# Optimization experiments

Hardware: AMD Instinct MI355X
Metric: run time of the kernel (lower is better)

## Reference

```python
import jax, jax.numpy as jnp
import numpy as np

D = 8  # polynomial degree; with bias present, basis has D columns (P1..PD)


def setup_inputs() -> dict:
    key = jax.random.key(0)
    k1, k2 = jax.random.split(key)
    batch, n_in, n_out = 65536, 256, 64
    x = jax.random.normal(k1, (batch, n_in), dtype=jnp.float32)
    c_basis = jax.random.normal(k2, (n_out, n_in, D), dtype=jnp.float32) * (1.0 / np.sqrt(n_in * D))
    bias = jnp.zeros((n_out,), dtype=jnp.float32)
    return {"x": x, "c_basis": c_basis, "bias": bias}


def _legendre_basis(x):
    # x: (batch, n_in). Returns (batch, n_in, D) = [P1(t), ..., PD(t)], t = tanh(x).
    t = jnp.tanh(x)
    p_prev = jnp.ones_like(t)  # P0
    p_curr = t                 # P1
    polys = [p_curr]
    for k in range(2, D + 1):  # small fixed-length loop over degree
        p_next = ((2 * k - 1) * t * p_curr - (k - 1) * p_prev) / k
        polys.append(p_next)
        p_prev, p_curr = p_curr, p_next
    return jnp.stack(polys, axis=-1)  # (batch, n_in, D)


def reference(x, c_basis, bias):
    # basis: (batch, n_in, D); contract over (n_in, D) with c_basis (n_out, n_in, D)
    leg = _legendre_basis(x)
    y = jnp.einsum('bid,oid->bo', leg, c_basis)
    return y + bias
```

## Files before the change

### kernel.cpp

```cpp
#include <hip/hip_runtime.h>
#include <hip/hip_bf16.h>

typedef _Float16 half2v __attribute__((ext_vector_type(2)));
typedef _Float16 half8 __attribute__((ext_vector_type(8)));
typedef __attribute__((ext_vector_type(4))) float floatx4;
typedef __attribute__((ext_vector_type(4))) unsigned int uintx4;

#define GLOBAL_AS __attribute__((address_space(1)))
#define LDS_AS __attribute__((address_space(3)))

__device__ __forceinline__ void async_ld16(const void* g, void* l) {
  __builtin_amdgcn_global_load_lds((const GLOBAL_AS unsigned int*)g,
                                   (LDS_AS unsigned int*)l, 16, 0, 0);
}

__device__ __forceinline__ half2v h2(float v) {
  return (half2v){(_Float16)v, (_Float16)v};
}

__device__ __forceinline__ void legendre2_f16(float xv0, float xv1,
                                              half8* fa0, half8* fa1) {
  float e0 = __builtin_amdgcn_exp2f(xv0 * 2.885390081777927f);
  float t0 = 1.0f - 2.0f * __builtin_amdgcn_rcpf(e0 + 1.0f);
  float e1 = __builtin_amdgcn_exp2f(xv1 * 2.885390081777927f);
  float t1 = 1.0f - 2.0f * __builtin_amdgcn_rcpf(e1 + 1.0f);
  half2v t;
  { auto tt = __builtin_amdgcn_cvt_pkrtz(t0, t1); __builtin_memcpy(&t, &tt, 4); }
  half2v p1 = t;
  half2v u2 = t * p1, w2 = u2 - h2(1.0f);  half2v p2 = h2(0.5f)      * w2 + u2;
  half2v u3 = t * p2, w3 = u3 - p1;        half2v p3 = h2(2.0f/3.0f) * w3 + u3;
  half2v u4 = t * p3, w4 = u4 - p2;        half2v p4 = h2(0.75f)     * w4 + u4;
  half2v u5 = t * p4, w5 = u5 - p3;        half2v p5 = h2(0.8f)      * w5 + u5;
  half2v u6 = t * p5, w6 = u6 - p4;        half2v p6 = h2(5.0f/6.0f) * w6 + u6;
  half2v u7 = t * p6, w7 = u7 - p5;        half2v p7 = h2(6.0f/7.0f) * w7 + u7;
  half2v u8 = t * p7, w8 = u8 - p6;        half2v p8 = h2(7.0f/8.0f) * w8 + u8;
  unsigned P[8];
  __builtin_memcpy(&P[0], &p1, 4); __builtin_memcpy(&P[1], &p2, 4);
  __builtin_memcpy(&P[2], &p3, 4); __builtin_memcpy(&P[3], &p4, 4);
  __builtin_memcpy(&P[4], &p5, 4); __builtin_memcpy(&P[5], &p6, 4);
  __builtin_memcpy(&P[6], &p7, 4); __builtin_memcpy(&P[7], &p8, 4);
  union { unsigned u[4]; half8 h; } a0, a1;
#pragma unroll
  for (int j = 0; j < 4; ++j) {
    a0.u[j] = __builtin_amdgcn_perm(P[2*j+1], P[2*j], 0x05040100u);
    a1.u[j] = __builtin_amdgcn_perm(P[2*j+1], P[2*j], 0x07060302u);
  }
  *fa0 = a0.h;
  *fa1 = a1.h;
}

__global__ void conv_kernel(const float* __restrict__ cb, _Float16* __restrict__ ws) {
  int t = blockIdx.x * 128 + threadIdx.x;
  int o = t >> 8;
  int i = t & 255;
  const floatx4* s = (const floatx4*)(cb + ((size_t)o * 256 + i) * 8);
  floatx4 v0 = s[0], v1 = s[1];
  union { _Float16 h[8]; uintx4 u; } w;
  w.h[0] = (_Float16)v0.x; w.h[1] = (_Float16)v0.y;
  w.h[2] = (_Float16)v0.z; w.h[3] = (_Float16)v0.w;
  w.h[4] = (_Float16)v1.x; w.h[5] = (_Float16)v1.y;
  w.h[6] = (_Float16)v1.z; w.h[7] = (_Float16)v1.w;
  *(uintx4*)(ws + (size_t)i * 512 + o * 8) = w.u;
}

#define NCH 16

__global__ __launch_bounds__(128, 2) void kan_kernel(
    const float* __restrict__ x, const _Float16* __restrict__ ws,
    const float* __restrict__ bias, float* __restrict__ y) {
  __shared__ __align__(16) _Float16 bt[2][16 * 64 * 8];

  const int tid  = threadIdx.x;
  const int wid  = tid >> 6;
  const int lane = tid & 63;
  const int m    = lane & 15;
  const int q    = lane >> 4;
  const int row_block = blockIdx.x * 64;

  floatx4 acc[2][4];
#pragma unroll
  for (int a = 0; a < 2; ++a)
#pragma unroll
    for (int nt = 0; nt < 4; ++nt) acc[a][nt] = (floatx4){0.f, 0.f, 0.f, 0.f};

  const _Float16* bsrc[8];
#pragma unroll
  for (int t = 0; t < 8; ++t)
    bsrc[t] = ws + (size_t)(t * 128 + wid * 64 + lane) * 8;

  const float* xp0 = x + (size_t)(row_block + wid * 32 + m) * 256 + q * 4;
  const float* xp1 = xp0 + 16 * 256;

  floatx4 xa0 = *(const floatx4*)xp0;
  floatx4 xa1 = *(const floatx4*)xp1;
  floatx4 xb0 = *(const floatx4*)(xp0 + 16);
  floatx4 xb1 = *(const floatx4*)(xp1 + 16);
  xp0 += 32; xp1 += 32;

  auto stage = [&](int b) {
#pragma unroll
    for (int t = 0; t < 8; ++t) {
      int sb = t * 128 + wid * 64;
      async_ld16(bsrc[t], &bt[b][sb * 8]);
      bsrc[t] += 8192;
    }
  };

  stage(0);

#pragma unroll 2
  for (int ch = 0; ch < NCH; ++ch) {
    const int buf = ch & 1;

    half8 f0[4], f1[4];
#pragma unroll
    for (int j = 0; j < 4; ++j)
      legendre2_f16(xa0[j], xa1[j], &f0[j], &f1[j]);

    asm volatile("s_barrier" ::: "memory");

    floatx4 xn0 = xb0, xn1 = xb1;
    if (ch + 1 < NCH) {
      stage(buf ^ 1);
      if (ch + 2 < NCH) {
        xn0 = *(const floatx4*)xp0;
        xn1 = *(const floatx4*)xp1;
        xp0 += 16; xp1 += 16;
      }
      asm volatile("s_waitcnt vmcnt(10)" ::: "memory");
    } else {
      asm volatile("s_waitcnt vmcnt(0)" ::: "memory");
    }
    asm volatile("s_barrier" ::: "memory");

    __builtin_amdgcn_s_setprio(1);
    const _Float16* bp = &bt[buf][q * 2048 + m * 8];
#pragma unroll
    for (int j = 0; j < 4; ++j) {
      half8 fb0 = *(const half8*)(bp + j * 512 + 0 * 128);
      half8 fb1 = *(const half8*)(bp + j * 512 + 1 * 128);
      half8 fb2 = *(const half8*)(bp + j * 512 + 2 * 128);
      half8 fb3 = *(const half8*)(bp + j * 512 + 3 * 128);
      acc[0][0] = __builtin_amdgcn_mfma_f32_16x16x32_f16(f0[j], fb0, acc[0][0], 0, 0, 0);
      acc[1][0] = __builtin_amdgcn_mfma_f32_16x16x32_f16(f1[j], fb0, acc[1][0], 0, 0, 0);
      acc[0][1] = __builtin_amdgcn_mfma_f32_16x16x32_f16(f0[j], fb1, acc[0][1], 0, 0, 0);
      acc[1][1] = __builtin_amdgcn_mfma_f32_16x16x32_f16(f1[j], fb1, acc[1][1], 0, 0, 0);
      acc[0][2] = __builtin_amdgcn_mfma_f32_16x16x32_f16(f0[j], fb2, acc[0][2], 0, 0, 0);
      acc[1][2] = __builtin_amdgcn_mfma_f32_16x16x32_f16(f1[j], fb2, acc[1][2], 0, 0, 0);
      acc[0][3] = __builtin_amdgcn_mfma_f32_16x16x32_f16(f0[j], fb3, acc[0][3], 0, 0, 0);
      acc[1][3] = __builtin_amdgcn_mfma_f32_16x16x32_f16(f1[j], fb3, acc[1][3], 0, 0, 0);
    }
    __builtin_amdgcn_s_setprio(0);

    xa0 = xb0; xa1 = xb1; xb0 = xn0; xb1 = xn1;
  }

  float bv[4];
#pragma unroll
  for (int nt = 0; nt < 4; ++nt) bv[nt] = bias[nt * 16 + m];
#pragma unroll
  for (int a = 0; a < 2; ++a) {
    int gr0 = row_block + wid * 32 + a * 16 + q * 4;
#pragma unroll
    for (int nt = 0; nt < 4; ++nt) {
#pragma unroll
      for (int r = 0; r < 4; ++r) {
        y[(size_t)(gr0 + r) * 64 + nt * 16 + m] = acc[a][nt][r] + bv[nt];
      }
    }
  }
}

extern "C" void kernel_launch(void* const* d_in, const int* in_sizes, int n_in,
                              void* d_out, int out_size, void* d_ws, size_t ws_size,
                              hipStream_t stream) {
  const float* x    = (const float*)d_in[0];
  const float* cb   = (const float*)d_in[1];
  const float* bias = (const float*)d_in[2];
  float* y = (float*)d_out;
  _Float16* ws = (_Float16*)d_ws;
  int batch = in_sizes[0] / 256;
  hipLaunchKernelGGL(conv_kernel, dim3(128), dim3(128), 0, stream, cb, ws);
  hipLaunchKernelGGL(kan_kernel, dim3(batch / 64), dim3(128), 0, stream, x, ws, bias, y);
}
```

Measured before the change: 121.4 us.

## Split K across two waves per block with per-wave LDS buffers and reduction

```diff
diff --git a/kernel.cpp b/kernel.cpp
--- a/kernel.cpp
+++ b/kernel.cpp
@@ -63,19 +63,17 @@
   *(uintx4*)(ws + (size_t)i * 512 + o * 8) = w.u;
 }
 
-#define NCH 16
-
-__global__ __launch_bounds__(128, 2) void kan_kernel(
+__global__ __launch_bounds__(128, 4) void kan_kernel(
     const float* __restrict__ x, const _Float16* __restrict__ ws,
     const float* __restrict__ bias, float* __restrict__ y) {
-  __shared__ __align__(16) _Float16 bt[2][16 * 64 * 8];
+  __shared__ __align__(16) _Float16 bt[2][2][2048];
 
   const int tid  = threadIdx.x;
   const int wid  = tid >> 6;
   const int lane = tid & 63;
   const int m    = lane & 15;
   const int q    = lane >> 4;
-  const int row_block = blockIdx.x * 64;
+  const int rb   = blockIdx.x * 32;
 
   floatx4 acc[2][4];
 #pragma unroll
@@ -83,89 +81,97 @@
 #pragma unroll
     for (int nt = 0; nt < 4; ++nt) acc[a][nt] = (floatx4){0.f, 0.f, 0.f, 0.f};
 
-  const _Float16* bsrc[8];
-#pragma unroll
-  for (int t = 0; t < 8; ++t)
-    bsrc[t] = ws + (size_t)(t * 128 + wid * 64 + lane) * 8;
+  const _Float16* bs0 = ws + (size_t)(wid * 128 +  0) * 512 + lane * 8;
+  const _Float16* bs1 = ws + (size_t)(wid * 128 + 32) * 512 + lane * 8;
+  const _Float16* bs2 = ws + (size_t)(wid * 128 + 64) * 512 + lane * 8;
+  const _Float16* bs3 = ws + (size_t)(wid * 128 + 96) * 512 + lane * 8;
 
-  const float* xp0 = x + (size_t)(row_block + wid * 32 + m) * 256 + q * 4;
+  const float* xp0 = x + (size_t)(rb + m) * 256 + wid * 128 + q * 32;
   const float* xp1 = xp0 + 16 * 256;
 
-  floatx4 xa0 = *(const floatx4*)xp0;
-  floatx4 xa1 = *(const floatx4*)xp1;
-  floatx4 xb0 = *(const floatx4*)(xp0 + 16);
-  floatx4 xb1 = *(const floatx4*)(xp1 + 16);
-  xp0 += 32; xp1 += 32;
+  floatx4 xs0[3], xs1[3];
+  xs0[0] = *(const floatx4*)(xp0);     xs1[0] = *(const floatx4*)(xp1);
+  xs0[1] = *(const floatx4*)(xp0 + 4); xs1[1] = *(const floatx4*)(xp1 + 4);
+  __builtin_amdgcn_sched_barrier(0);
 
-  auto stage = [&](int b) {
-#pragma unroll
-    for (int t = 0; t < 8; ++t) {
-      int sb = t * 128 + wid * 64;
-      async_ld16(bsrc[t], &bt[b][sb * 8]);
-      bsrc[t] += 8192;
-    }
-  };
+  {
+    _Float16* ld = &bt[wid][0][0];
+    async_ld16(bs0, ld);        async_ld16(bs1, ld + 512);
+    async_ld16(bs2, ld + 1024); async_ld16(bs3, ld + 1536);
+    bs0 += 512; bs1 += 512; bs2 += 512; bs3 += 512;
+  }
+  __builtin_amdgcn_sched_barrier(0);
 
-  stage(0);
-
-#pragma unroll 2
-  for (int ch = 0; ch < NCH; ++ch) {
-    const int buf = ch & 1;
-
-    half8 f0[4], f1[4];
-#pragma unroll
-    for (int j = 0; j < 4; ++j)
-      legendre2_f16(xa0[j], xa1[j], &f0[j], &f1[j]);
-
-    asm volatile("s_barrier" ::: "memory");
-
-    floatx4 xn0 = xb0, xn1 = xb1;
-    if (ch + 1 < NCH) {
-      stage(buf ^ 1);
-      if (ch + 2 < NCH) {
-        xn0 = *(const floatx4*)xp0;
-        xn1 = *(const floatx4*)xp1;
-        xp0 += 16; xp1 += 16;
-      }
-      asm volatile("s_waitcnt vmcnt(10)" ::: "memory");
-    } else {
-      asm volatile("s_waitcnt vmcnt(0)" ::: "memory");
-    }
-    asm volatile("s_barrier" ::: "memory");
-
-    __builtin_amdgcn_s_setprio(1);
-    const _Float16* bp = &bt[buf][q * 2048 + m * 8];
-#pragma unroll
-    for (int j = 0; j < 4; ++j) {
-      half8 fb0 = *(const half8*)(bp + j * 512 + 0 * 128);
-      half8 fb1 = *(const half8*)(bp + j * 512 + 1 * 128);
-      half8 fb2 = *(const half8*)(bp + j * 512 + 2 * 128);
-      half8 fb3 = *(const half8*)(bp + j * 512 + 3 * 128);
-      acc[0][0] = __builtin_amdgcn_mfma_f32_16x16x32_f16(f0[j], fb0, acc[0][0], 0, 0, 0);
-      acc[1][0] = __builtin_amdgcn_mfma_f32_16x16x32_f16(f1[j], fb0, acc[1][0], 0, 0, 0);
-      acc[0][1] = __builtin_amdgcn_mfma_f32_16x16x32_f16(f0[j], fb1, acc[0][1], 0, 0, 0);
-      acc[1][1] = __builtin_amdgcn_mfma_f32_16x16x32_f16(f1[j], fb1, acc[1][1], 0, 0, 0);
-      acc[0][2] = __builtin_amdgcn_mfma_f32_16x16x32_f16(f0[j], fb2, acc[0][2], 0, 0, 0);
-      acc[1][2] = __builtin_amdgcn_mfma_f32_16x16x32_f16(f1[j], fb2, acc[1][2], 0, 0, 0);
-      acc[0][3] = __builtin_amdgcn_mfma_f32_16x16x32_f16(f0[j], fb3, acc[0][3], 0, 0, 0);
-      acc[1][3] = __builtin_amdgcn_mfma_f32_16x16x32_f16(f1[j], fb3, acc[1][3], 0, 0, 0);
-    }
-    __builtin_amdgcn_s_setprio(0);
-
-    xa0 = xb0; xa1 = xb1; xb0 = xn0; xb1 = xn1;
+#define CHUNK(ch, N, DOX)                                                      \
+  {                                                                            \
+    if constexpr (DOX) {                                                       \
+      constexpr int gp = (ch) / 4 + 2;                                         \
+      xs0[gp % 3] = *(const floatx4*)(xp0 + gp * 4);                           \
+      xs1[gp % 3] = *(const floatx4*)(xp1 + gp * 4);                           \
+    }                                                                          \
+    __builtin_amdgcn_sched_barrier(0);                                         \
+    if constexpr ((ch) < 31) {                                                 \
+      _Float16* ld = &bt[wid][((ch) + 1) & 1][0];                              \
+      async_ld16(bs0, ld);        async_ld16(bs1, ld + 512);                   \
+      async_ld16(bs2, ld + 1024); async_ld16(bs3, ld + 1536);                  \
+      bs0 += 512; bs1 += 512; bs2 += 512; bs3 += 512;                          \
+    }                                                                          \
+    __builtin_amdgcn_sched_barrier(0);                                         \
+    half8 f0, f1;                                                              \
+    legendre2_f16(xs0[((ch) / 4) % 3][(ch) % 4],                               \
+                  xs1[((ch) / 4) % 3][(ch) % 4], &f0, &f1);                    \
+    asm volatile("s_waitcnt vmcnt(" #N ")" ::: "memory");                      \
+    const _Float16* bp = &bt[wid][(ch) & 1][q * 512 + m * 8];                  \
+    half8 fb0 = *(const half8*)(bp + 0);                                       \
+    half8 fb1 = *(const half8*)(bp + 128);                                     \
+    half8 fb2 = *(const half8*)(bp + 256);                                     \
+    half8 fb3 = *(const half8*)(bp + 384);                                     \
+    __builtin_amdgcn_s_setprio(1);                                             \
+    acc[0][0] = __builtin_amdgcn_mfma_f32_16x16x32_f16(f0, fb0, acc[0][0], 0, 0, 0); \
+    acc[1][0] = __builtin_amdgcn_mfma_f32_16x16x32_f16(f1, fb0, acc[1][0], 0, 0, 0); \
+    acc[0][1] = __builtin_amdgcn_mfma_f32_16x16x32_f16(f0, fb1, acc[0][1], 0, 0, 0); \
+    acc[1][1] = __builtin_amdgcn_mfma_f32_16x16x32_f16(f1, fb1, acc[1][1], 0, 0, 0); \
+    acc[0][2] = __builtin_amdgcn_mfma_f32_16x16x32_f16(f0, fb2, acc[0][2], 0, 0, 0); \
+    acc[1][2] = __builtin_amdgcn_mfma_f32_16x16x32_f16(f1, fb2, acc[1][2], 0, 0, 0); \
+    acc[0][3] = __builtin_amdgcn_mfma_f32_16x16x32_f16(f0, fb3, acc[0][3], 0, 0, 0); \
+    acc[1][3] = __builtin_amdgcn_mfma_f32_16x16x32_f16(f1, fb3, acc[1][3], 0, 0, 0); \
+    __builtin_amdgcn_s_setprio(0);                                             \
   }
 
-  float bv[4];
+  CHUNK(0, 6, 1)  CHUNK(1, 4, 0)  CHUNK(2, 4, 0)  CHUNK(3, 4, 0)
+  CHUNK(4, 6, 1)  CHUNK(5, 4, 0)  CHUNK(6, 4, 0)  CHUNK(7, 4, 0)
+  CHUNK(8, 6, 1)  CHUNK(9, 4, 0)  CHUNK(10, 4, 0) CHUNK(11, 4, 0)
+  CHUNK(12, 6, 1) CHUNK(13, 4, 0) CHUNK(14, 4, 0) CHUNK(15, 4, 0)
+  CHUNK(16, 6, 1) CHUNK(17, 4, 0) CHUNK(18, 4, 0) CHUNK(19, 4, 0)
+  CHUNK(20, 6, 1) CHUNK(21, 4, 0) CHUNK(22, 4, 0) CHUNK(23, 4, 0)
+  CHUNK(24, 4, 0) CHUNK(25, 4, 0) CHUNK(26, 4, 0) CHUNK(27, 4, 0)
+  CHUNK(28, 4, 0) CHUNK(29, 4, 0) CHUNK(30, 4, 0) CHUNK(31, 0, 0)
+#undef CHUNK
+
+  float* red = (float*)&bt[0][0][0];
+  __syncthreads();
+  if (wid) {
 #pragma unroll
-  for (int nt = 0; nt < 4; ++nt) bv[nt] = bias[nt * 16 + m];
+    for (int a = 0; a < 2; ++a)
 #pragma unroll
-  for (int a = 0; a < 2; ++a) {
-    int gr0 = row_block + wid * 32 + a * 16 + q * 4;
+      for (int nt = 0; nt < 4; ++nt)
+        *(floatx4*)(red + ((a * 4 + nt) * 64 + lane) * 4) = acc[a][nt];
+  }
+  __syncthreads();
+  if (!wid) {
+    float bv[4];
 #pragma unroll
-    for (int nt = 0; nt < 4; ++nt) {
+    for (int nt = 0; nt < 4; ++nt) bv[nt] = bias[nt * 16 + m];
 #pragma unroll
-      for (int r = 0; r < 4; ++r) {
-        y[(size_t)(gr0 + r) * 64 + nt * 16 + m] = acc[a][nt][r] + bv[nt];
+    for (int a = 0; a < 2; ++a) {
+      int gr0 = rb + a * 16 + q * 4;
+#pragma unroll
+      for (int nt = 0; nt < 4; ++nt) {
+        floatx4 p = *(const floatx4*)(red + ((a * 4 + nt) * 64 + lane) * 4);
+#pragma unroll
+        for (int r = 0; r < 4; ++r) {
+          y[(size_t)(gr0 + r) * 64 + nt * 16 + m] = acc[a][nt][r] + p[r] + bv[nt];
+        }
       }
     }
   }
@@ -181,5 +187,5 @@
   _Float16* ws = (_Float16*)d_ws;
   int batch = in_sizes[0] / 256;
   hipLaunchKernelGGL(conv_kernel, dim3(128), dim3(128), 0, stream, cb, ws);
-  hipLaunchKernelGGL(kan_kernel, dim3(batch / 64), dim3(128), 0, stream, x, ws, bias, y);
+  hipLaunchKernelGGL(kan_kernel, dim3(batch / 32), dim3(128), 0, stream, x, ws, bias, y);
 }
```

Result: slower. 136.0 us (+12.1%).

## Split K across waves, stage x via async LDS loads, reduce partials in LDS

Applied to the files above, without the earlier changes.

```diff
diff --git a/kernel.cpp b/kernel.cpp
--- a/kernel.cpp
+++ b/kernel.cpp
@@ -63,19 +63,22 @@
   *(uintx4*)(ws + (size_t)i * 512 + o * 8) = w.u;
 }
 
-#define NCH 16
+#define NSTEP 16
 
-__global__ __launch_bounds__(128, 2) void kan_kernel(
+__global__ __launch_bounds__(256, 4) void kan_kernel(
     const float* __restrict__ x, const _Float16* __restrict__ ws,
     const float* __restrict__ bias, float* __restrict__ y) {
-  __shared__ __align__(16) _Float16 bt[2][16 * 64 * 8];
+  __shared__ __align__(16) _Float16 bt[2][8192];
+  __shared__ __align__(16) float xs[2][1024];
 
   const int tid  = threadIdx.x;
   const int wid  = tid >> 6;
+  const int kh   = wid >> 1;
+  const int rh   = wid & 1;
   const int lane = tid & 63;
   const int m    = lane & 15;
   const int q    = lane >> 4;
-  const int row_block = blockIdx.x * 64;
+  const int rb   = blockIdx.x * 64;
 
   floatx4 acc[2][4];
 #pragma unroll
@@ -83,89 +86,97 @@
 #pragma unroll
     for (int nt = 0; nt < 4; ++nt) acc[a][nt] = (floatx4){0.f, 0.f, 0.f, 0.f};
 
-  const _Float16* bsrc[8];
+  const _Float16* bsrc[4];
 #pragma unroll
-  for (int t = 0; t < 8; ++t)
-    bsrc[t] = ws + (size_t)(t * 128 + wid * 64 + lane) * 8;
+  for (int j = 0; j < 4; ++j) {
+    int t = wid * 4 + j;
+    bsrc[j] = ws + (size_t)((t >> 3) * 128 + (t & 7)) * 512 + lane * 8;
+  }
 
-  const float* xp0 = x + (size_t)(row_block + wid * 32 + m) * 256 + q * 4;
-  const float* xp1 = xp0 + 16 * 256;
-
-  floatx4 xa0 = *(const floatx4*)xp0;
-  floatx4 xa1 = *(const floatx4*)xp1;
-  floatx4 xb0 = *(const floatx4*)(xp0 + 16);
-  floatx4 xb1 = *(const floatx4*)(xp1 + 16);
-  xp0 += 32; xp1 += 32;
+  const float* xsrc;
+  {
+    int u = wid * 64 + lane;
+    int row = u >> 2;
+    int p = (u & 3) ^ ((row >> 1) & 3);
+    xsrc = x + (size_t)(rb + row) * 256 + (p >> 1) * 128 + (p & 1) * 4;
+  }
 
   auto stage = [&](int b) {
 #pragma unroll
-    for (int t = 0; t < 8; ++t) {
-      int sb = t * 128 + wid * 64;
-      async_ld16(bsrc[t], &bt[b][sb * 8]);
-      bsrc[t] += 8192;
+    for (int j = 0; j < 4; ++j) {
+      async_ld16(bsrc[j], &bt[b][(wid * 4 + j) * 512]);
+      bsrc[j] += 8 * 512;
     }
+    async_ld16(xsrc, &xs[b][wid * 256]);
+    xsrc += 8;
   };
 
   stage(0);
 
+  const int row0 = rh * 32 + m;
+  const int sw   = (row0 >> 1) & 3;
+
 #pragma unroll 2
-  for (int ch = 0; ch < NCH; ++ch) {
+  for (int ch = 0; ch < NSTEP; ++ch) {
     const int buf = ch & 1;
-
-    half8 f0[4], f1[4];
-#pragma unroll
-    for (int j = 0; j < 4; ++j)
-      legendre2_f16(xa0[j], xa1[j], &f0[j], &f1[j]);
-
     asm volatile("s_barrier" ::: "memory");
-
-    floatx4 xn0 = xb0, xn1 = xb1;
-    if (ch + 1 < NCH) {
+    if (ch + 1 < NSTEP) {
       stage(buf ^ 1);
-      if (ch + 2 < NCH) {
-        xn0 = *(const floatx4*)xp0;
-        xn1 = *(const floatx4*)xp1;
-        xp0 += 16; xp1 += 16;
-      }
-      asm volatile("s_waitcnt vmcnt(10)" ::: "memory");
+      asm volatile("s_waitcnt vmcnt(5)" ::: "memory");
     } else {
       asm volatile("s_waitcnt vmcnt(0)" ::: "memory");
     }
     asm volatile("s_barrier" ::: "memory");
 
-    __builtin_amdgcn_s_setprio(1);
-    const _Float16* bp = &bt[buf][q * 2048 + m * 8];
 #pragma unroll
-    for (int j = 0; j < 4; ++j) {
-      half8 fb0 = *(const half8*)(bp + j * 512 + 0 * 128);
-      half8 fb1 = *(const half8*)(bp + j * 512 + 1 * 128);
-      half8 fb2 = *(const half8*)(bp + j * 512 + 2 * 128);
-      half8 fb3 = *(const half8*)(bp + j * 512 + 3 * 128);
-      acc[0][0] = __builtin_amdgcn_mfma_f32_16x16x32_f16(f0[j], fb0, acc[0][0], 0, 0, 0);
-      acc[1][0] = __builtin_amdgcn_mfma_f32_16x16x32_f16(f1[j], fb0, acc[1][0], 0, 0, 0);
-      acc[0][1] = __builtin_amdgcn_mfma_f32_16x16x32_f16(f0[j], fb1, acc[0][1], 0, 0, 0);
-      acc[1][1] = __builtin_amdgcn_mfma_f32_16x16x32_f16(f1[j], fb1, acc[1][1], 0, 0, 0);
-      acc[0][2] = __builtin_amdgcn_mfma_f32_16x16x32_f16(f0[j], fb2, acc[0][2], 0, 0, 0);
-      acc[1][2] = __builtin_amdgcn_mfma_f32_16x16x32_f16(f1[j], fb2, acc[1][2], 0, 0, 0);
-      acc[0][3] = __builtin_amdgcn_mfma_f32_16x16x32_f16(f0[j], fb3, acc[0][3], 0, 0, 0);
-      acc[1][3] = __builtin_amdgcn_mfma_f32_16x16x32_f16(f1[j], fb3, acc[1][3], 0, 0, 0);
+    for (int ks = 0; ks < 2; ++ks) {
+      const int xi = row0 * 16 + (((kh * 2 + ks) ^ sw) << 2) + q;
+      float xv0 = xs[buf][xi];
+      float xv1 = xs[buf][xi + 256];
+      half8 f0, f1;
+      legendre2_f16(xv0, xv1, &f0, &f1);
+      const _Float16* bp = &bt[buf][(kh * 8 + ks * 4 + q) * 512 + m * 8];
+      half8 fb0 = *(const half8*)(bp + 0);
+      half8 fb1 = *(const half8*)(bp + 128);
+      half8 fb2 = *(const half8*)(bp + 256);
+      half8 fb3 = *(const half8*)(bp + 384);
+      __builtin_amdgcn_s_setprio(1);
+      acc[0][0] = __builtin_amdgcn_mfma_f32_16x16x32_f16(f0, fb0, acc[0][0], 0, 0, 0);
+      acc[1][0] = __builtin_amdgcn_mfma_f32_16x16x32_f16(f1, fb0, acc[1][0], 0, 0, 0);
+      acc[0][1] = __builtin_amdgcn_mfma_f32_16x16x32_f16(f0, fb1, acc[0][1], 0, 0, 0);
+      acc[1][1] = __builtin_amdgcn_mfma_f32_16x16x32_f16(f1, fb1, acc[1][1], 0, 0, 0);
+      acc[0][2] = __builtin_amdgcn_mfma_f32_16x16x32_f16(f0, fb2, acc[0][2], 0, 0, 0);
+      acc[1][2] = __builtin_amdgcn_mfma_f32_16x16x32_f16(f1, fb2, acc[1][2], 0, 0, 0);
+      acc[0][3] = __builtin_amdgcn_mfma_f32_16x16x32_f16(f0, fb3, acc[0][3], 0, 0, 0);
+      acc[1][3] = __builtin_amdgcn_mfma_f32_16x16x32_f16(f1, fb3, acc[1][3], 0, 0, 0);
+      __builtin_amdgcn_s_setprio(0);
     }
-    __builtin_amdgcn_s_setprio(0);
-
-    xa0 = xb0; xa1 = xb1; xb0 = xn0; xb1 = xn1;
   }
 
-  float bv[4];
+  float* red = (float*)&bt[0][0];
+  __syncthreads();
+  if (kh) {
 #pragma unroll
-  for (int nt = 0; nt < 4; ++nt) bv[nt] = bias[nt * 16 + m];
+    for (int a = 0; a < 2; ++a)
 #pragma unroll
-  for (int a = 0; a < 2; ++a) {
-    int gr0 = row_block + wid * 32 + a * 16 + q * 4;
+      for (int nt = 0; nt < 4; ++nt)
+        *(floatx4*)(red + ((rh * 8 + a * 4 + nt) * 64 + lane) * 4) = acc[a][nt];
+  }
+  __syncthreads();
+  if (!kh) {
+    float bv[4];
 #pragma unroll
-    for (int nt = 0; nt < 4; ++nt) {
+    for (int nt = 0; nt < 4; ++nt) bv[nt] = bias[nt * 16 + m];
 #pragma unroll
-      for (int r = 0; r < 4; ++r) {
-        y[(size_t)(gr0 + r) * 64 + nt * 16 + m] = acc[a][nt][r] + bv[nt];
+    for (int a = 0; a < 2; ++a) {
+      int gr0 = rb + rh * 32 + a * 16 + q * 4;
+#pragma unroll
+      for (int nt = 0; nt < 4; ++nt) {
+        floatx4 p = *(const floatx4*)(red + ((rh * 8 + a * 4 + nt) * 64 + lane) * 4);
+#pragma unroll
+        for (int r = 0; r < 4; ++r) {
+          y[(size_t)(gr0 + r) * 64 + nt * 16 + m] = acc[a][nt][r] + p[r] + bv[nt];
+        }
       }
     }
   }
@@ -181,5 +192,5 @@
   _Float16* ws = (_Float16*)d_ws;
   int batch = in_sizes[0] / 256;
   hipLaunchKernelGGL(conv_kernel, dim3(128), dim3(128), 0, stream, cb, ws);
-  hipLaunchKernelGGL(kan_kernel, dim3(batch / 64), dim3(128), 0, stream, x, ws, bias, y);
+  hipLaunchKernelGGL(kan_kernel, dim3(batch / 64), dim3(256), 0, stream, x, ws, bias, y);
 }
```

Result: faster. 118.7 us (-2.2%).
